# Optimization experiments

Measured on AMD Instinct MI355X. Metric: run time of the kernel, lower is better.

Reference implementation:

```python
import jax, jax.numpy as jnp
import numpy as np

NUM_HEADS = 16
HEAD_DIM = 80
HIDDEN = 1280
SEQ = 3072
NUM_SEGS = 6  # 6 packed images of 512 patches each


def rotate_half(x):
    x1, x2 = jnp.split(x, 2, axis=-1)
    return jnp.concatenate([-x2, x1], axis=-1)


def setup_inputs() -> dict:
    key = jax.random.key(0)
    ks = jax.random.split(key, 6)
    hidden_states = jax.random.normal(ks[0], (SEQ, HIDDEN), dtype=jnp.float32)
    # RoPE tables as in Qwen-VL vision: freqs over half the head_dim, duplicated
    half = HEAD_DIM // 2
    inv_freq = 1.0 / (10000.0 ** (jnp.arange(half, dtype=jnp.float32) / half))
    pos = jnp.arange(SEQ, dtype=jnp.float32)[:, None]
    freqs = pos * inv_freq[None, :]                      # (SEQ, half)
    emb = jnp.concatenate([freqs, freqs], axis=-1)       # (SEQ, HEAD_DIM)
    cos = jnp.cos(emb)
    sin = jnp.sin(emb)
    # Packed segment boundaries: [0, 512, 1024, ..., 3072]
    cu_seqlens = jnp.arange(0, SEQ + 1, SEQ // NUM_SEGS, dtype=jnp.int32)
    scale = 0.02
    w_qkv = jax.random.normal(ks[1], (3 * HIDDEN, HIDDEN), dtype=jnp.float32) * scale
    b_qkv = jax.random.normal(ks[2], (3 * HIDDEN,), dtype=jnp.float32) * scale
    w_proj = jax.random.normal(ks[3], (HIDDEN, HIDDEN), dtype=jnp.float32) * scale
    b_proj = jax.random.normal(ks[4], (HIDDEN,), dtype=jnp.float32) * scale
    return {
        "hidden_states": hidden_states, "cos": cos, "sin": sin,
        "w_qkv": w_qkv, "b_qkv": b_qkv, "w_proj": w_proj, "b_proj": b_proj,
        "cu_seqlens": cu_seqlens,
    }


def reference(hidden_states, cos, sin, w_qkv, b_qkv, w_proj, b_proj, cu_seqlens):
    S, H = hidden_states.shape
    nh, hd = NUM_HEADS, H // NUM_HEADS

    # Fused QKV projection: (S, 3H) -> q, k, v each (S, nh, hd)
    qkv = hidden_states @ w_qkv.T + b_qkv
    qkv = qkv.reshape(S, 3, nh, hd)
    q, k, v = qkv[:, 0], qkv[:, 1], qkv[:, 2]

    # Inline RoPE on q/k (cos/sin broadcast over heads)
    c = cos[:, None, :]
    s = sin[:, None, :]
    q = q * c + rotate_half(q) * s
    k = k * c + rotate_half(k) * s

    # Original casts fp32 -> fp16 for the flash attention kernel
    q16 = q.astype(jnp.float16)
    k16 = k.astype(jnp.float16)
    v16 = v.astype(jnp.float16)

    # Varlen masking: tokens attend only within their own packed segment
    tok = jnp.arange(S)
    seg = jnp.searchsorted(cu_seqlens, tok, side="right")  # (S,)
    same_seg = seg[:, None] == seg[None, :]                 # (S, S)

    scale = hd ** (-0.5)
    # Scores accumulated in fp32 (as flash attention does internally)
    scores = jnp.einsum("qhd,khd->hqk", q16, k16,
                        preferred_element_type=jnp.float32) * scale
    scores = jnp.where(same_seg[None], scores, jnp.finfo(jnp.float32).min)
    weights = jax.nn.softmax(scores, axis=-1).astype(jnp.float16)  # (nh, S, S)

    attn = jnp.einsum("hqk,khd->qhd", weights, v16)  # (S, nh, hd) fp16
    attn = attn.astype(jnp.float32).reshape(S, H)
    return attn @ w_proj.T + b_proj
```

## Files before the change

### kernel.cpp

```cpp
#include <hip/hip_runtime.h>

typedef _Float16 f16;
typedef _Float16 half8 __attribute__((ext_vector_type(8)));
typedef _Float16 half4 __attribute__((ext_vector_type(4)));
typedef float f32x4 __attribute__((ext_vector_type(4)));

__device__ __forceinline__ void gld_lds16(const void* g, void* l) {
  __builtin_amdgcn_global_load_lds((const __attribute__((address_space(1))) void*)g,
                                   (__attribute__((address_space(3))) void*)l, 16, 0, 0);
}

template <int CTRL>
__device__ __forceinline__ float dppf(float x) {
  return __builtin_bit_cast(float,
      __builtin_amdgcn_mov_dpp(__builtin_bit_cast(int, x), CTRL, 0xf, 0xf, true));
}
__device__ __forceinline__ float dpp_max16(float v) {
  v = fmaxf(v, dppf<0xB1>(v));
  v = fmaxf(v, dppf<0x4E>(v));
  v = fmaxf(v, dppf<0x128>(v));
  v = fmaxf(v, dppf<0x140>(v));
  return v;
}
__device__ __forceinline__ float dpp_sum16(float v) {
  v += dppf<0xB1>(v);
  v += dppf<0x4E>(v);
  v += dppf<0x128>(v);
  v += dppf<0x140>(v);
  return v;
}

__global__ void cvt_all(const float* __restrict__ hid, const float* __restrict__ wq,
                        const float* __restrict__ wp, f16* __restrict__ hid16,
                        f16* __restrict__ wq16, f16* __restrict__ wp16) {
  int b = blockIdx.x;
  const float* in;
  f16* out;
  int i;
  if (b < 3840) { in = hid; out = hid16; i = b * 256 + threadIdx.x; }
  else if (b < 8640) { in = wq; out = wq16; i = (b - 3840) * 256 + threadIdx.x; }
  else { in = wp; out = wp16; i = (b - 8640) * 256 + threadIdx.x; }
  float4 v = ((const float4*)in)[i];
  half4 o;
  o.x = (f16)v.x; o.y = (f16)v.y; o.z = (f16)v.z; o.w = (f16)v.w;
  ((half4*)out)[i] = o;
}

template <bool OUT_F16>
__global__ __launch_bounds__(256, 2) void gemm_bt(const f16* __restrict__ A,
                                                  const f16* __restrict__ B,
                                                  const float* __restrict__ bias,
                                                  void* __restrict__ Cout,
                                                  int K, int lda, int ldb, int ldc) {
  __shared__ f16 As[128 * 32];
  __shared__ f16 Bs[128 * 32];
  const int tid = threadIdx.x, lane = tid & 63, wave = tid >> 6;
  const int bm = blockIdx.x * 128, bn = blockIdx.y * 128;
  const int wm = (wave & 1) * 64, wn = (wave >> 1) * 64;
  const int lm = lane & 15, kq = (lane >> 4) * 8;
  const int arow = tid >> 2, acol = (tid & 3) * 8;

  const f16* Ab = A + (size_t)(bm + arow) * lda + acol;
  const f16* Bb = B + (size_t)(bn + arow) * ldb + acol;
  f16* AsW = As + wave * 512;
  f16* BsW = Bs + wave * 512;

  f32x4 acc[4][4] = {};
  for (int k0 = 0; k0 < K; k0 += 32) {
    gld_lds16(Ab + k0, AsW);
    gld_lds16(Ab + (size_t)64 * lda + k0, AsW + 2048);
    gld_lds16(Bb + k0, BsW);
    gld_lds16(Bb + (size_t)64 * ldb + k0, BsW + 2048);
    __syncthreads();
    half8 af[4], bf[4];
#pragma unroll
    for (int mt = 0; mt < 4; mt++) af[mt] = *(const half8*)&As[(wm + 16 * mt + lm) * 32 + kq];
#pragma unroll
    for (int nt = 0; nt < 4; nt++) bf[nt] = *(const half8*)&Bs[(wn + 16 * nt + lm) * 32 + kq];
#pragma unroll
    for (int mt = 0; mt < 4; mt++)
#pragma unroll
      for (int nt = 0; nt < 4; nt++)
        acc[mt][nt] = __builtin_amdgcn_mfma_f32_16x16x32_f16(af[mt], bf[nt], acc[mt][nt], 0, 0, 0);
    __syncthreads();
  }
  const int q4 = lane >> 4;
#pragma unroll
  for (int mt = 0; mt < 4; mt++)
#pragma unroll
    for (int nt = 0; nt < 4; nt++)
#pragma unroll
      for (int r = 0; r < 4; r++) {
        int gr = bm + wm + 16 * mt + 4 * q4 + r;
        int gc = bn + wn + 16 * nt + lm;
        float v = acc[mt][nt][r] + bias[gc];
        if (OUT_F16)
          ((f16*)Cout)[(size_t)gr * ldc + gc] = (f16)v;
        else
          ((float*)Cout)[(size_t)gr * ldc + gc] = v;
      }
}

template <bool OUT_F16>
__global__ __launch_bounds__(256, 2) void gemm_bt64(const f16* __restrict__ A,
                                                    const f16* __restrict__ B,
                                                    const float* __restrict__ bias,
                                                    void* __restrict__ Cout,
                                                    int K, int lda, int ldb, int ldc) {
  __shared__ f16 As[64 * 32];
  __shared__ f16 Bs[128 * 32];
  const int tid = threadIdx.x, lane = tid & 63, wave = tid >> 6;
  const int bm = blockIdx.x * 64, bn = blockIdx.y * 128;
  const int wm = (wave & 1) * 32, wn = (wave >> 1) * 64;
  const int lm = lane & 15, kq = (lane >> 4) * 8;
  const int arow = tid >> 2, acol = (tid & 3) * 8;

  const f16* Ab = A + (size_t)(bm + arow) * lda + acol;
  const f16* Bb = B + (size_t)(bn + arow) * ldb + acol;
  f16* AsW = As + wave * 512;
  f16* BsW = Bs + wave * 512;

  f32x4 acc[2][4] = {};
  for (int k0 = 0; k0 < K; k0 += 32) {
    gld_lds16(Ab + k0, AsW);
    gld_lds16(Bb + k0, BsW);
    gld_lds16(Bb + (size_t)64 * ldb + k0, BsW + 2048);
    __syncthreads();
    half8 af[2], bf[4];
#pragma unroll
    for (int mt = 0; mt < 2; mt++) af[mt] = *(const half8*)&As[(wm + 16 * mt + lm) * 32 + kq];
#pragma unroll
    for (int nt = 0; nt < 4; nt++) bf[nt] = *(const half8*)&Bs[(wn + 16 * nt + lm) * 32 + kq];
#pragma unroll
    for (int mt = 0; mt < 2; mt++)
#pragma unroll
      for (int nt = 0; nt < 4; nt++)
        acc[mt][nt] = __builtin_amdgcn_mfma_f32_16x16x32_f16(af[mt], bf[nt], acc[mt][nt], 0, 0, 0);
    __syncthreads();
  }
  const int q4 = lane >> 4;
#pragma unroll
  for (int mt = 0; mt < 2; mt++)
#pragma unroll
    for (int nt = 0; nt < 4; nt++)
#pragma unroll
      for (int r = 0; r < 4; r++) {
        int gr = bm + wm + 16 * mt + 4 * q4 + r;
        int gc = bn + wn + 16 * nt + lm;
        float v = acc[mt][nt][r] + bias[gc];
        if (OUT_F16)
          ((f16*)Cout)[(size_t)gr * ldc + gc] = (f16)v;
        else
          ((float*)Cout)[(size_t)gr * ldc + gc] = v;
      }
}

__global__ void rope_transpose(f16* __restrict__ qkv, const float* __restrict__ cosb,
                               const float* __restrict__ sinb, f16* __restrict__ vt) {
  __shared__ f16 tile[64][72];
  const int b = blockIdx.x;
  if (b < 1920) {
    int idx = b * 256 + threadIdx.x;
    int c = idx % 5;
    int t = idx / 5;
    int h = t % 16; t /= 16;
    int qk = t & 1;
    int s = t >> 1;
    size_t base = (size_t)s * 3840 + qk * 1280 + h * 80 + c * 8;
    half8 x = *(half8*)&qkv[base];
    half8 y = *(half8*)&qkv[base + 40];
    const float* cp = cosb + s * 80 + c * 8;
    const float* sp = sinb + s * 80 + c * 8;
    half8 ox, oy;
#pragma unroll
    for (int i = 0; i < 8; i++) {
      float cs = cp[i], sn = sp[i];
      float xf = (float)x[i], yf = (float)y[i];
      ox[i] = (f16)(xf * cs - yf * sn);
      oy[i] = (f16)(yf * cs + xf * sn);
    }
    *(half8*)&qkv[base] = ox;
    *(half8*)&qkv[base + 40] = oy;
  } else {
    const int bb = b - 1920;
    const int bs = (bb % 48) * 64;
    const int bd = (bb / 48) * 64;
    const int r = threadIdx.x >> 2, c = (threadIdx.x & 3) * 16;
    *(uint4*)&tile[r][c] = *(const uint4*)&qkv[(size_t)(bs + r) * 3840 + 2560 + bd + c];
    *(uint4*)&tile[r][c + 8] = *(const uint4*)&qkv[(size_t)(bs + r) * 3840 + 2560 + bd + c + 8];
    __syncthreads();
    f16 tmp[16];
#pragma unroll
    for (int i = 0; i < 16; i++) tmp[i] = tile[c + i][r];
    *(uint4*)&vt[(size_t)(bd + r) * 3072 + bs + c] = *(uint4*)&tmp[0];
    *(uint4*)&vt[(size_t)(bd + r) * 3072 + bs + c + 8] = *(uint4*)&tmp[8];
  }
}

__global__ __launch_bounds__(256, 4) void flash_attn5(const f16* __restrict__ qkv,
                                                      const f16* __restrict__ vt,
                                                      f16* __restrict__ attn) {
  __shared__ f16 S[20480];
  f16* Ks = S;
  f16* Vs = S + 10240;
  const int tid = threadIdx.x, lane = tid & 63, wave = tid >> 6;
  const int lm = lane & 15, q4 = lane >> 4;
  const int h = blockIdx.x, g = blockIdx.z;
  const int qbase = g * 512 + blockIdx.y * 64 + wave * 16;
  f16* P = S + wave * 2112;
  const half8 hz = {};

  const f16* qrow = qkv + (size_t)(qbase + lm) * 3840 + h * 80;
  half8 qf[3];
  qf[0] = *(const half8*)(qrow + q4 * 8);
  qf[1] = *(const half8*)(qrow + 32 + q4 * 8);
  qf[2] = (q4 < 2) ? *(const half8*)(qrow + 64 + q4 * 8) : hz;

  size_t kgo[5], vgo[5];
#pragma unroll
  for (int i = 0; i < 5; i++) {
    int t = (wave * 5 + i) * 1024 + lane * 16;
    int kr = t / 160, kcb = t % 160;
    kgo[i] = (size_t)(g * 512 + kr) * 3840 + 1280 + h * 80 + (kcb >> 1);
    int vd = t >> 8, vsb = t & 255;
    vgo[i] = (size_t)(h * 80 + vd) * 3072 + g * 512 + (vsb >> 1);
  }

  f32x4 oacc[5] = {};
  float mprev[4] = {-1e30f, -1e30f, -1e30f, -1e30f};
  float lsum[4] = {0.f, 0.f, 0.f, 0.f};
  const float sc = 0.11180339887498949f * 1.4426950408889634f;

  for (int j = 0; j < 4; j++) {
    __syncthreads();
#pragma unroll
    for (int i = 0; i < 5; i++) {
      int chunk = wave * 5 + i;
      gld_lds16(qkv + kgo[i] + (size_t)j * (128 * 3840), Ks + chunk * 512);
      gld_lds16(vt + vgo[i] + j * 128, Vs + chunk * 512);
    }
    __syncthreads();

    f32x4 sacc[8] = {};
#pragma unroll
    for (int ks = 0; ks < 3; ks++) {
      half8 bk[8];
#pragma unroll
      for (int nt = 0; nt < 8; nt++)
        bk[nt] = (ks < 2 || q4 < 2)
                     ? *(const half8*)&Ks[(16 * nt + lm) * 80 + 32 * ks + q4 * 8]
                     : hz;
#pragma unroll
      for (int nt = 0; nt < 8; nt++)
        sacc[nt] = __builtin_amdgcn_mfma_f32_16x16x32_f16(qf[ks], bk[nt], sacc[nt], 0, 0, 0);
    }

    float mnew[4], alpha[4], rs[4];
#pragma unroll
    for (int r = 0; r < 4; r++) {
      float v = fmaxf(fmaxf(fmaxf(sacc[0][r], sacc[1][r]), fmaxf(sacc[2][r], sacc[3][r])),
                      fmaxf(fmaxf(sacc[4][r], sacc[5][r]), fmaxf(sacc[6][r], sacc[7][r])));
      v = dpp_max16(v);
      mnew[r] = fmaxf(mprev[r], v * sc);
      alpha[r] = __builtin_exp2f(mprev[r] - mnew[r]);
      mprev[r] = mnew[r];
      rs[r] = 0.f;
    }
#pragma unroll
    for (int nt = 0; nt < 8; nt++)
#pragma unroll
      for (int r = 0; r < 4; r++) {
        float p = __builtin_exp2f(sacc[nt][r] * sc - mnew[r]);
        sacc[nt][r] = p;
        rs[r] += p;
      }
#pragma unroll
    for (int r = 0; r < 4; r++) {
      float v = dpp_sum16(rs[r]);
      lsum[r] = alpha[r] * lsum[r] + v;
#pragma unroll
      for (int nt2 = 0; nt2 < 5; nt2++) oacc[nt2][r] *= alpha[r];
    }

    __syncthreads();
#pragma unroll
    for (int nt = 0; nt < 8; nt++)
#pragma unroll
      for (int r = 0; r < 4; r++)
        P[(4 * q4 + r) * 132 + 16 * nt + lm] = (f16)sacc[nt][r];

#pragma unroll
    for (int ks = 0; ks < 4; ks++) {
      half8 ap = *(const half8*)&P[lm * 132 + ks * 32 + q4 * 8];
      half8 bv[5];
#pragma unroll
      for (int nt2 = 0; nt2 < 5; nt2++)
        bv[nt2] = *(const half8*)&Vs[(16 * nt2 + lm) * 128 + ks * 32 + q4 * 8];
#pragma unroll
      for (int nt2 = 0; nt2 < 5; nt2++)
        oacc[nt2] = __builtin_amdgcn_mfma_f32_16x16x32_f16(ap, bv[nt2], oacc[nt2], 0, 0, 0);
    }
  }
#pragma unroll
  for (int r = 0; r < 4; r++) {
    float inv = 1.0f / lsum[r];
    int s = qbase + 4 * q4 + r;
#pragma unroll
    for (int nt2 = 0; nt2 < 5; nt2++)
      attn[(size_t)s * 1280 + h * 80 + 16 * nt2 + lm] = (f16)(oacc[nt2][r] * inv);
  }
}

extern "C" void kernel_launch(void* const* d_in, const int* in_sizes, int n_in,
                              void* d_out, int out_size, void* d_ws, size_t ws_size,
                              hipStream_t stream) {
  const float* hidden = (const float*)d_in[0];
  const float* cosb   = (const float*)d_in[1];
  const float* sinb   = (const float*)d_in[2];
  const float* w_qkv  = (const float*)d_in[3];
  const float* b_qkv  = (const float*)d_in[4];
  const float* w_proj = (const float*)d_in[5];
  const float* b_proj = (const float*)d_in[6];

  char* ws = (char*)d_ws;
  f16* hidden16 = (f16*)(ws + 0);
  f16* wqkv16   = (f16*)(ws + 7864320);
  f16* wproj16  = (f16*)(ws + 17694720);
  f16* qkv16    = (f16*)(ws + 20971520);
  f16* attn16   = (f16*)(ws + 44564480);
  f16* vt16     = hidden16;

  cvt_all<<<10240, 256, 0, stream>>>(hidden, w_qkv, w_proj, hidden16, wqkv16, wproj16);

  gemm_bt<true><<<dim3(24, 30), 256, 0, stream>>>(hidden16, wqkv16, b_qkv, qkv16,
                                                  1280, 1280, 1280, 3840);

  rope_transpose<<<2880, 256, 0, stream>>>(qkv16, cosb, sinb, vt16);

  flash_attn5<<<dim3(16, 8, 6), 256, 0, stream>>>(qkv16, vt16, attn16);

  gemm_bt64<false><<<dim3(48, 10), 256, 0, stream>>>(attn16, wproj16, b_proj, d_out,
                                                     1280, 1280, 1280, 1280);
}
```

Baseline: 211.0 us.

## Store GEMM tiles in LDS in MFMA fragment order and double K-step

Both GEMM kernels now load global tiles directly into LDS in the exact per-lane MFMA fragment order, so each wave reads its operand fragments as contiguous lane*8 half8 loads instead of row-strided ones that may bank-conflict. The K loop also moves from 32 to 64 elements per iteration, halving the number of barriers per tile at the cost of double the LDS footprint. Global reads become 16-row by 8-half chunks per lane, which may reduce coalescing per instruction.

```diff
diff --git a/kernel.cpp b/kernel.cpp
--- a/kernel.cpp
+++ b/kernel.cpp
@@ -52,39 +52,48 @@
                                                   const float* __restrict__ bias,
                                                   void* __restrict__ Cout,
                                                   int K, int lda, int ldb, int ldc) {
-  __shared__ f16 As[128 * 32];
-  __shared__ f16 Bs[128 * 32];
+  __shared__ f16 As[16 * 512];
+  __shared__ f16 Bs[16 * 512];
   const int tid = threadIdx.x, lane = tid & 63, wave = tid >> 6;
+  const int lm = lane & 15, q4 = lane >> 4;
   const int bm = blockIdx.x * 128, bn = blockIdx.y * 128;
-  const int wm = (wave & 1) * 64, wn = (wave >> 1) * 64;
-  const int lm = lane & 15, kq = (lane >> 4) * 8;
-  const int arow = tid >> 2, acol = (tid & 3) * 8;
-
-  const f16* Ab = A + (size_t)(bm + arow) * lda + acol;
-  const f16* Bb = B + (size_t)(bn + arow) * ldb + acol;
-  f16* AsW = As + wave * 512;
-  f16* BsW = Bs + wave * 512;
+  const int wm2 = wave & 1, wn2 = wave >> 1;
+
+  const f16* asrc[4];
+  const f16* bsrc[4];
+#pragma unroll
+  for (int i = 0; i < 4; i++) {
+    int c = wave * 4 + i;
+    int w2 = c >> 3, t = (c >> 1) & 3, ks = c & 1;
+    asrc[i] = A + (size_t)(bm + w2 * 64 + t * 16 + lm) * lda + ks * 32 + q4 * 8;
+    bsrc[i] = B + (size_t)(bn + w2 * 64 + t * 16 + lm) * ldb + ks * 32 + q4 * 8;
+  }
 
   f32x4 acc[4][4] = {};
-  for (int k0 = 0; k0 < K; k0 += 32) {
-    gld_lds16(Ab + k0, AsW);
-    gld_lds16(Ab + (size_t)64 * lda + k0, AsW + 2048);
-    gld_lds16(Bb + k0, BsW);
-    gld_lds16(Bb + (size_t)64 * ldb + k0, BsW + 2048);
-    __syncthreads();
-    half8 af[4], bf[4];
-#pragma unroll
-    for (int mt = 0; mt < 4; mt++) af[mt] = *(const half8*)&As[(wm + 16 * mt + lm) * 32 + kq];
-#pragma unroll
-    for (int nt = 0; nt < 4; nt++) bf[nt] = *(const half8*)&Bs[(wn + 16 * nt + lm) * 32 + kq];
-#pragma unroll
-    for (int mt = 0; mt < 4; mt++)
+  for (int k0 = 0; k0 < K; k0 += 64) {
+#pragma unroll
+    for (int i = 0; i < 4; i++) gld_lds16(asrc[i] + k0, As + (wave * 4 + i) * 512);
+#pragma unroll
+    for (int i = 0; i < 4; i++) gld_lds16(bsrc[i] + k0, Bs + (wave * 4 + i) * 512);
+    __syncthreads();
+#pragma unroll
+    for (int ks = 0; ks < 2; ks++) {
+      half8 af[4], bf[4];
+#pragma unroll
+      for (int mt = 0; mt < 4; mt++)
+        af[mt] = *(const half8*)&As[((wm2 * 4 + mt) * 2 + ks) * 512 + lane * 8];
 #pragma unroll
       for (int nt = 0; nt < 4; nt++)
-        acc[mt][nt] = __builtin_amdgcn_mfma_f32_16x16x32_f16(af[mt], bf[nt], acc[mt][nt], 0, 0, 0);
-    __syncthreads();
-  }
-  const int q4 = lane >> 4;
+        bf[nt] = *(const half8*)&Bs[((wn2 * 4 + nt) * 2 + ks) * 512 + lane * 8];
+#pragma unroll
+      for (int mt = 0; mt < 4; mt++)
+#pragma unroll
+        for (int nt = 0; nt < 4; nt++)
+          acc[mt][nt] = __builtin_amdgcn_mfma_f32_16x16x32_f16(af[mt], bf[nt], acc[mt][nt], 0, 0, 0);
+    }
+    __syncthreads();
+  }
+  const int wm = wm2 * 64, wn = wn2 * 64;
 #pragma unroll
   for (int mt = 0; mt < 4; mt++)
 #pragma unroll
@@ -107,38 +116,51 @@
                                                     const float* __restrict__ bias,
                                                     void* __restrict__ Cout,
                                                     int K, int lda, int ldb, int ldc) {
-  __shared__ f16 As[64 * 32];
-  __shared__ f16 Bs[128 * 32];
+  __shared__ f16 Sm[24 * 512];
   const int tid = threadIdx.x, lane = tid & 63, wave = tid >> 6;
+  const int lm = lane & 15, q4 = lane >> 4;
   const int bm = blockIdx.x * 64, bn = blockIdx.y * 128;
-  const int wm = (wave & 1) * 32, wn = (wave >> 1) * 64;
-  const int lm = lane & 15, kq = (lane >> 4) * 8;
-  const int arow = tid >> 2, acol = (tid & 3) * 8;
-
-  const f16* Ab = A + (size_t)(bm + arow) * lda + acol;
-  const f16* Bb = B + (size_t)(bn + arow) * ldb + acol;
-  f16* AsW = As + wave * 512;
-  f16* BsW = Bs + wave * 512;
+  const int wm2 = wave & 1, wn2 = wave >> 1;
+
+  const f16* src[6];
+  f16* dst[6];
+#pragma unroll
+  for (int i = 0; i < 6; i++) {
+    int c = wave * 6 + i;
+    if (c < 8) {
+      int w2 = c >> 2, t = (c >> 1) & 1, ks = c & 1;
+      src[i] = A + (size_t)(bm + w2 * 32 + t * 16 + lm) * lda + ks * 32 + q4 * 8;
+    } else {
+      int cb = c - 8;
+      int w2 = cb >> 3, nt = (cb >> 1) & 3, ks = cb & 1;
+      src[i] = B + (size_t)(bn + w2 * 64 + nt * 16 + lm) * ldb + ks * 32 + q4 * 8;
+    }
+    dst[i] = Sm + c * 512;
+  }
 
   f32x4 acc[2][4] = {};
-  for (int k0 = 0; k0 < K; k0 += 32) {
-    gld_lds16(Ab + k0, AsW);
-    gld_lds16(Bb + k0, BsW);
-    gld_lds16(Bb + (size_t)64 * ldb + k0, BsW + 2048);
-    __syncthreads();
-    half8 af[2], bf[4];
-#pragma unroll
-    for (int mt = 0; mt < 2; mt++) af[mt] = *(const half8*)&As[(wm + 16 * mt + lm) * 32 + kq];
-#pragma unroll
-    for (int nt = 0; nt < 4; nt++) bf[nt] = *(const half8*)&Bs[(wn + 16 * nt + lm) * 32 + kq];
-#pragma unroll
-    for (int mt = 0; mt < 2; mt++)
+  for (int k0 = 0; k0 < K; k0 += 64) {
+#pragma unroll
+    for (int i = 0; i < 6; i++) gld_lds16(src[i] + k0, dst[i]);
+    __syncthreads();
+#pragma unroll
+    for (int ks = 0; ks < 2; ks++) {
+      half8 af[2], bf[4];
+#pragma unroll
+      for (int mt = 0; mt < 2; mt++)
+        af[mt] = *(const half8*)&Sm[((wm2 * 2 + mt) * 2 + ks) * 512 + lane * 8];
 #pragma unroll
       for (int nt = 0; nt < 4; nt++)
-        acc[mt][nt] = __builtin_amdgcn_mfma_f32_16x16x32_f16(af[mt], bf[nt], acc[mt][nt], 0, 0, 0);
-    __syncthreads();
-  }
-  const int q4 = lane >> 4;
+        bf[nt] = *(const half8*)&Sm[(8 + (wn2 * 4 + nt) * 2 + ks) * 512 + lane * 8];
+#pragma unroll
+      for (int mt = 0; mt < 2; mt++)
+#pragma unroll
+        for (int nt = 0; nt < 4; nt++)
+          acc[mt][nt] = __builtin_amdgcn_mfma_f32_16x16x32_f16(af[mt], bf[nt], acc[mt][nt], 0, 0, 0);
+    }
+    __syncthreads();
+  }
+  const int wm = wm2 * 32, wn = wn2 * 64;
 #pragma unroll
   for (int mt = 0; mt < 2; mt++)
 #pragma unroll
```

After: 243.9 us. +15.6%, slower.
